# Kernel tuning notes

Measured on AMD Instinct MI355X. Metric: run time of the kernel, lower is better.

Reference implementation:

```python
import jax, jax.numpy as jnp
import numpy as np
from jax import lax

B, S, D = 2, 4096, 1024
E, H, K = 8, 2816, 2  # hidden_dim 4096 -> int(2*4096/3)=2730 -> round up to multiple_of 256 -> 2816


def setup_inputs() -> dict:
    key = jax.random.key(0)
    ks = jax.random.split(key, 5)
    scale = 0.02
    return {
        "x": jax.random.normal(ks[0], (B, S, D), dtype=jnp.float32),
        "router_w": jax.random.normal(ks[1], (E, D), dtype=jnp.float32) * scale,
        "w1": jax.random.normal(ks[2], (E, D, H), dtype=jnp.float32) * scale,
        "w2": jax.random.normal(ks[3], (E, H, D), dtype=jnp.float32) * scale,
        "w3": jax.random.normal(ks[4], (E, D, H), dtype=jnp.float32) * scale,
        "top_k": K,
    }


def reference(x, router_w, w1, w2, w3, top_k):
    b, s, d = x.shape
    e = router_w.shape[0]
    xf = x.reshape(-1, d)                                # [T, D]
    logits = xf @ router_w.T                             # [T, E]
    vals, idx = lax.top_k(logits, top_k)                 # [T, K]
    rw = jax.nn.softmax(vals.astype(jnp.float32), axis=-1).astype(x.dtype)  # [T, K]
    # combine[t, e] = routing weight of expert e for token t (0 if not selected)
    combine = jnp.sum(jax.nn.one_hot(idx, e, dtype=x.dtype) * rw[..., None], axis=1)  # [T, E]

    def body(acc, ew):
        w1e, w2e, w3e, ce = ew                           # [D,H], [H,D], [D,H], [T]
        h = jax.nn.silu(xf @ w1e) * (xf @ w3e)           # SwiGLU FFN, [T, H]
        return acc + (h @ w2e) * ce[:, None], None

    out, _ = lax.scan(body, jnp.zeros_like(xf), (w1, w2, w3, combine.T))
    return out.reshape(b, s, d)
```

## Files before the change

kernel.cpp:

```cpp
#include <hip/hip_runtime.h>
#include <stdint.h>

#define T_TOK 8192
#define DIM   1024
#define NE    8
#define NH    2816
#define NROWS (T_TOK*2)

typedef __attribute__((ext_vector_type(8))) __bf16 bf16x8;
typedef __attribute__((ext_vector_type(4))) float  f32x4;
typedef __attribute__((ext_vector_type(8))) unsigned short ushort8;

typedef __attribute__((address_space(1))) const unsigned int g_as1;
typedef __attribute__((address_space(3))) unsigned int l_as3;
#define GLL(g, l) __builtin_amdgcn_global_load_lds((g_as1*)(g), (l_as3*)(l), 16, 0, 0)
#define MFMA16(a,b,c) __builtin_amdgcn_mfma_f32_16x16x32_bf16(a,b,c,0,0,0)

__device__ __forceinline__ unsigned short f2bf(float f){
  union { float f; uint32_t u; } v; v.f = f;
  uint32_t r = (v.u + 0x7FFFu + ((v.u >> 16) & 1u)) >> 16;
  return (unsigned short)r;
}


__global__ void zero_init_k(float4* __restrict__ out, int* counts, int* cursor){
  if (blockIdx.x == 0 && threadIdx.x < NE){ counts[threadIdx.x] = 0; cursor[threadIdx.x] = 0; }
  int i = blockIdx.x*blockDim.x + threadIdx.x;
  const int n4 = T_TOK*DIM/4;
  const float4 z = make_float4(0.f,0.f,0.f,0.f);
  for (; i < n4; i += gridDim.x*blockDim.x) out[i] = z;
}

__global__ void cvt_k(const float* __restrict__ x, unsigned short* __restrict__ xbf){
  int i = blockIdx.x*blockDim.x + threadIdx.x;
  const int total = T_TOK*DIM/8;
  for (; i < total; i += gridDim.x*blockDim.x){
    const float4 a = *(const float4*)(x + (size_t)i*8);
    const float4 b = *(const float4*)(x + (size_t)i*8 + 4);
    ushort4 lo = make_ushort4(f2bf(a.x), f2bf(a.y), f2bf(a.z), f2bf(a.w));
    ushort4 hi = make_ushort4(f2bf(b.x), f2bf(b.y), f2bf(b.z), f2bf(b.w));
    *(ushort4*)(xbf + (size_t)i*8)     = lo;
    *(ushort4*)(xbf + (size_t)i*8 + 4) = hi;
  }
}


__global__ __launch_bounds__(256) void transpA_k(
    const float* __restrict__ w1, const float* __restrict__ w3,
    const float* __restrict__ w2,
    unsigned short* __restrict__ w1t, unsigned short* __restrict__ w3t,
    unsigned short* __restrict__ w2t, int zbase)
{
  __shared__ unsigned short Tl[64*72];
  const int z = zbase + blockIdx.y;
  const int f = blockIdx.x;
  const size_t DS = (size_t)DIM*NH;
  const float* src; unsigned short* dst; int R, C, rt, ct;
  if (z < 16){
    R = DIM; C = NH; rt = f/44; ct = f - rt*44;
    const int e = z & 7;
    src = (z < 8 ? w1 : w3) + (size_t)e*DS;
    dst = (z < 8 ? w1t : w3t) + (size_t)e*DS;
  } else {
    R = NH; C = DIM; rt = f/16; ct = f - rt*16;
    const int e = z - 16;
    src = w2 + (size_t)e*DS;
    dst = w2t + (size_t)e*DS;
  }
  const int r0 = rt*64, c0 = ct*64;
  const int t = threadIdx.x;
  #pragma unroll
  for (int i=0;i<4;i++){
    const int r  = (t>>4) + i*16;
    const int cq = t & 15;
    const float4 v = *(const float4*)(src + (size_t)(r0+r)*C + c0 + cq*4);
    Tl[(cq*4+0)*72 + r] = f2bf(v.x);
    Tl[(cq*4+1)*72 + r] = f2bf(v.y);
    Tl[(cq*4+2)*72 + r] = f2bf(v.z);
    Tl[(cq*4+3)*72 + r] = f2bf(v.w);
  }
  __syncthreads();
  #pragma unroll
  for (int i=0;i<2;i++){
    const int c  = i*32 + (t>>3);
    const int r8 = (t&7)*8;
    const ushort8 v = *(const ushort8*)&Tl[c*72 + r8];
    *(ushort8*)(dst + (size_t)(c0+c)*R + r0 + r8) = v;
  }
}


__global__ void router_k(const float* __restrict__ x, const float* __restrict__ rw,
                         unsigned short* __restrict__ xbf,
                         int* __restrict__ topk_e, float* __restrict__ topk_w,
                         int* __restrict__ counts){
  const int t = blockIdx.x;
  const int l = threadIdx.x;
  const float* xr = x + (size_t)t * DIM;
  unsigned short* xo = xbf + (size_t)t * DIM;
  float acc[NE];
  #pragma unroll
  for (int e=0;e<NE;e++) acc[e] = 0.f;
  #pragma unroll
  for (int i=0;i<4;i++){
    const int idx = l*4 + i*256;
    const float4 xv = *(const float4*)(xr + idx);
    ushort4 pk = make_ushort4(f2bf(xv.x), f2bf(xv.y), f2bf(xv.z), f2bf(xv.w));
    *(ushort4*)(xo + idx) = pk;
    #pragma unroll
    for (int e=0;e<NE;e++){
      const float4 wv = *(const float4*)(rw + e*DIM + idx);
      acc[e] += xv.x*wv.x + xv.y*wv.y + xv.z*wv.z + xv.w*wv.w;
    }
  }
  #pragma unroll
  for (int e=0;e<NE;e++){
    float v = acc[e];
    #pragma unroll
    for (int off=32; off; off>>=1) v += __shfl_xor(v, off);
    acc[e] = v;
  }
  if (l == 0){
    int e0 = 0; float v0 = acc[0];
    #pragma unroll
    for (int e=1;e<NE;e++) if (acc[e] > v0){ v0 = acc[e]; e0 = e; }
    int e1 = -1; float v1 = -1e30f;
    #pragma unroll
    for (int e=0;e<NE;e++) if (e != e0 && acc[e] > v1){ v1 = acc[e]; e1 = e; }
    float ex = __expf(v1 - v0);
    float s  = 1.f + ex;
    topk_e[t*2]   = e0;  topk_e[t*2+1] = e1;
    topk_w[t*2]   = 1.f/s; topk_w[t*2+1] = ex/s;
    atomicAdd(&counts[e0], 1);
    atomicAdd(&counts[e1], 1);
  }
}

__global__ void prefix_k(const int* __restrict__ counts, int* __restrict__ offs){
  if (threadIdx.x == 0 && blockIdx.x == 0){
    int s = 0;
    for (int e=0;e<NE;e++){ offs[e] = s; s += counts[e]; }
  }
}

__global__ void scatter_k(const int* __restrict__ topk_e, const float* __restrict__ topk_w,
                          const int* __restrict__ offs, int* __restrict__ cursor,
                          int* __restrict__ row_tok, float* __restrict__ row_w){
  int t = blockIdx.x*blockDim.x + threadIdx.x;
  if (t >= T_TOK) return;
  #pragma unroll
  for (int k=0;k<2;k++){
    int e = topk_e[t*2+k];
    int p = atomicAdd(&cursor[e], 1);
    int flat = offs[e] + p;
    row_tok[flat] = t;
    row_w[flat]   = topk_w[t*2+k];
  }
}


__global__ __launch_bounds__(512,2) void gemm1_p(
    const unsigned short* __restrict__ xbf,
    const unsigned short* __restrict__ w1t, const unsigned short* __restrict__ w3t,
    unsigned short* __restrict__ hbuf,
    const int* __restrict__ row_tok,
    const int* __restrict__ counts, const int* __restrict__ offs)
{
  __shared__ unsigned short As [3][128*32];
  __shared__ unsigned short B1s[3][128*32];
  __shared__ unsigned short B3s[3][128*32];

  const int i   = blockIdx.y*64 + blockIdx.x;
  const int lid = (i & 7)*1408 + (i >> 3);
  const int e   = lid / 1408;
  const int rem = lid - e*1408;
  const int h0  = (rem >> 6) * 128;
  const int rb  = rem & 63;

  const int cnt = counts[e];
  const int row0 = rb * 128;
  if (row0 >= cnt) return;
  const int nv   = min(128, cnt - row0);
  const int base = offs[e] + row0;
  const int NK   = DIM/32;

  const int t = threadIdx.x;
  const int r_loc = t >> 2, sct = t & 3;
  const int csw = (sct ^ ((r_loc >> 1) & 3)) * 8;
  const int tok = row_tok[base + min(r_loc, nv-1)];
  const unsigned short* aS  = xbf + (size_t)tok*DIM + csw;
  const unsigned short* b1S = w1t + ((size_t)(e*NH + h0) + r_loc)*DIM + csw;
  const unsigned short* b3S = w3t + ((size_t)(e*NH + h0) + r_loc)*DIM + csw;
  const int lo = t*16;

  const int wid = t >> 6, l = t & 63;
  const int wr = wid >> 2, wc = wid & 3;
  const int lr = l & 15,  lk = l >> 4;
  const int rc = (lk ^ ((lr >> 1) & 3)) * 8;

  f32x4 acc1[4][2], acc3[4][2];
  #pragma unroll
  for (int m=0;m<4;m++)
    #pragma unroll
    for (int n=0;n<2;n++){ acc1[m][n] = (f32x4)0.f; acc3[m][n] = (f32x4)0.f; }

  GLL(aS,    (char*)As[0]+lo); GLL(b1S,    (char*)B1s[0]+lo); GLL(b3S,    (char*)B3s[0]+lo);
  GLL(aS+32, (char*)As[1]+lo); GLL(b1S+32, (char*)B1s[1]+lo); GLL(b3S+32, (char*)B3s[1]+lo);

  for (int kt=0; kt<NK; ++kt){
    if (kt < NK-1) asm volatile("s_waitcnt vmcnt(3)" ::: "memory");
    else           asm volatile("s_waitcnt vmcnt(0)" ::: "memory");
    __builtin_amdgcn_s_barrier();

    if (kt+2 < NK){
      const int kA = (kt+2)*32;
      char* ad  = (char*)As [(kt+2)%3];
      char* b1d = (char*)B1s[(kt+2)%3];
      char* b3d = (char*)B3s[(kt+2)%3];
      GLL(aS+kA, ad+lo); GLL(b1S+kA, b1d+lo); GLL(b3S+kA, b3d+lo);
    }

    const unsigned short* Ab  = As [kt%3];
    const unsigned short* B1b = B1s[kt%3];
    const unsigned short* B3b = B3s[kt%3];

    bf16x8 a[4], b1[2], b3[2];
    #pragma unroll
    for (int m=0;m<4;m++) a[m] = *(const bf16x8*)&Ab[(wr*64 + m*16 + lr)*32 + rc];
    #pragma unroll
    for (int n=0;n<2;n++){
      b1[n] = *(const bf16x8*)&B1b[(wc*32 + n*16 + lr)*32 + rc];
      b3[n] = *(const bf16x8*)&B3b[(wc*32 + n*16 + lr)*32 + rc];
    }
    __builtin_amdgcn_s_setprio(1);
    #pragma unroll
    for (int m=0;m<4;m++)
      #pragma unroll
      for (int n=0;n<2;n++){
        acc1[m][n] = MFMA16(a[m], b1[n], acc1[m][n]);
        acc3[m][n] = MFMA16(a[m], b3[n], acc3[m][n]);
      }
    __builtin_amdgcn_s_setprio(0);
  }

  #pragma unroll
  for (int m=0;m<4;m++){
    #pragma unroll
    for (int i2=0;i2<4;i2++){
      const int r = wr*64 + m*16 + lk*4 + i2;
      if (r < nv){
        const size_t rowbase = (size_t)(base + r) * NH;
        #pragma unroll
        for (int n=0;n<2;n++){
          float z  = acc1[m][n][i2];
          float p3 = acc3[m][n][i2];
          float hv = (z / (1.f + __expf(-z))) * p3;
          hbuf[rowbase + h0 + wc*32 + n*16 + lr] = f2bf(hv);
        }
      }
    }
  }
}

__global__ __launch_bounds__(512,2) void gemm2_p(
    const unsigned short* __restrict__ hbuf,
    const unsigned short* __restrict__ w2t,
    float* __restrict__ out,
    const int* __restrict__ row_tok, const float* __restrict__ row_w,
    const int* __restrict__ counts, const int* __restrict__ offs)
{
  __shared__ unsigned short As[3][128*32];
  __shared__ unsigned short Bs[3][128*32];

  const int i   = blockIdx.y*64 + blockIdx.x;
  const int lid = (i & 7)*512 + (i >> 3);
  const int e   = lid >> 9;
  const int rem = lid & 511;
  const int d0  = (rem >> 6) * 128;
  const int rb  = rem & 63;

  const int cnt = counts[e];
  const int row0 = rb * 128;
  if (row0 >= cnt) return;
  const int nv   = min(128, cnt - row0);
  const int base = offs[e] + row0;
  const int NK   = NH/32;

  const int t = threadIdx.x;
  const int r_loc = t >> 2, sct = t & 3;
  const int csw = (sct ^ ((r_loc >> 1) & 3)) * 8;
  const unsigned short* aS = hbuf + (size_t)(base + min(r_loc, nv-1))*NH + csw;
  const unsigned short* bS = w2t + ((size_t)(e*DIM + d0) + r_loc)*NH + csw;
  const int lo = t*16;

  const int wid = t >> 6, l = t & 63;
  const int wr = wid >> 2, wc = wid & 3;
  const int lr = l & 15,  lk = l >> 4;
  const int rc = (lk ^ ((lr >> 1) & 3)) * 8;

  f32x4 acc[4][2];
  #pragma unroll
  for (int m=0;m<4;m++)
    #pragma unroll
    for (int n=0;n<2;n++) acc[m][n] = (f32x4)0.f;

  GLL(aS,    (char*)As[0]+lo); GLL(bS,    (char*)Bs[0]+lo);
  GLL(aS+32, (char*)As[1]+lo); GLL(bS+32, (char*)Bs[1]+lo);

  for (int kt=0; kt<NK; ++kt){
    if (kt < NK-1) asm volatile("s_waitcnt vmcnt(2)" ::: "memory");
    else           asm volatile("s_waitcnt vmcnt(0)" ::: "memory");
    __builtin_amdgcn_s_barrier();

    if (kt+2 < NK){
      const int kA = (kt+2)*32;
      char* ad = (char*)As[(kt+2)%3];
      char* bd = (char*)Bs[(kt+2)%3];
      GLL(aS+kA, ad+lo); GLL(bS+kA, bd+lo);
    }

    const unsigned short* Ab = As[kt%3];
    const unsigned short* Bb = Bs[kt%3];

    bf16x8 a[4], b[2];
    #pragma unroll
    for (int m=0;m<4;m++) a[m] = *(const bf16x8*)&Ab[(wr*64 + m*16 + lr)*32 + rc];
    #pragma unroll
    for (int n=0;n<2;n++)  b[n] = *(const bf16x8*)&Bb[(wc*32 + n*16 + lr)*32 + rc];
    __builtin_amdgcn_s_setprio(1);
    #pragma unroll
    for (int m=0;m<4;m++)
      #pragma unroll
      for (int n=0;n<2;n++)
        acc[m][n] = MFMA16(a[m], b[n], acc[m][n]);
    __builtin_amdgcn_s_setprio(0);
  }

  #pragma unroll
  for (int m=0;m<4;m++){
    #pragma unroll
    for (int i2=0;i2<4;i2++){
      const int r = wr*64 + m*16 + lk*4 + i2;
      if (r < nv){
        const int flat = base + r;
        const int tok  = row_tok[flat];
        const float wgt = row_w[flat];
        float* orow = out + (size_t)tok * DIM + d0 + wc*32;
        #pragma unroll
        for (int n=0;n<2;n++)
          atomicAdd(&orow[n*16 + lr], acc[m][n][i2] * wgt);
      }
    }
  }
}


__global__ __launch_bounds__(256) void gemm1_k(
    const unsigned short* __restrict__ xbf,
    const float* __restrict__ w1, const float* __restrict__ w3,
    unsigned short* __restrict__ hbuf,
    const int* __restrict__ row_tok,
    const int* __restrict__ counts, const int* __restrict__ offs)
{
  __shared__ unsigned short Al [128*32];
  __shared__ unsigned short B1l[128*32];
  __shared__ unsigned short B3l[128*32];
  const int e   = blockIdx.y >> 6;
  const int rb  = blockIdx.y & 63;
  const int cnt = counts[e];
  const int row0 = rb * 128;
  if (row0 >= cnt) return;
  const int nv   = min(128, cnt - row0);
  const int base = offs[e] + row0;
  const int h0   = blockIdx.x * 128;
  const int t  = threadIdx.x;
  const int ar0 = t >> 2;
  const int ac  = t & 3;
  const int tok0 = row_tok[base + min(ar0,      nv-1)];
  const int tok1 = row_tok[base + min(ar0 + 64, nv-1)];
  const size_t asrc0 = (size_t)tok0 * DIM + ac*8;
  const size_t asrc1 = (size_t)tok1 * DIM + ac*8;
  const int dg = t >> 5;
  const int hq = t & 31;
  const float* w1p = w1 + (size_t)e * DIM * NH + (size_t)(h0 + hq*4);
  const float* w3p = w3 + (size_t)e * DIM * NH + (size_t)(h0 + hq*4);
  const int wid = t >> 6, l = t & 63;
  const int wr = wid >> 1, wc = wid & 1;
  const int lr = l & 15,  lk = l >> 4;
  f32x4 acc1[4][4], acc3[4][4];
  #pragma unroll
  for (int m=0;m<4;m++)
    #pragma unroll
    for (int n=0;n<4;n++){ acc1[m][n] = (f32x4)0.f; acc3[m][n] = (f32x4)0.f; }
  for (int kk=0; kk<DIM/32; ++kk){
    const int k0 = kk*32;
    __syncthreads();
    *(uint4*)&Al[ar0*32 + ac*8]      = *(const uint4*)(xbf + asrc0 + k0);
    *(uint4*)&Al[(ar0+64)*32 + ac*8] = *(const uint4*)(xbf + asrc1 + k0);
    {
      const float4 f0 = *(const float4*)(w1p + (size_t)(k0 + dg*4 + 0)*NH);
      const float4 f1 = *(const float4*)(w1p + (size_t)(k0 + dg*4 + 1)*NH);
      const float4 f2 = *(const float4*)(w1p + (size_t)(k0 + dg*4 + 2)*NH);
      const float4 f3 = *(const float4*)(w1p + (size_t)(k0 + dg*4 + 3)*NH);
      const float* p0=(const float*)&f0; const float* p1=(const float*)&f1;
      const float* p2=(const float*)&f2; const float* p3=(const float*)&f3;
      #pragma unroll
      for (int j=0;j<4;j++){
        ushort4 pk = make_ushort4(f2bf(p0[j]), f2bf(p1[j]), f2bf(p2[j]), f2bf(p3[j]));
        *(ushort4*)&B1l[(hq*4+j)*32 + dg*4] = pk;
      }
      const float4 g0 = *(const float4*)(w3p + (size_t)(k0 + dg*4 + 0)*NH);
      const float4 g1 = *(const float4*)(w3p + (size_t)(k0 + dg*4 + 1)*NH);
      const float4 g2 = *(const float4*)(w3p + (size_t)(k0 + dg*4 + 2)*NH);
      const float4 g3 = *(const float4*)(w3p + (size_t)(k0 + dg*4 + 3)*NH);
      const float* q0=(const float*)&g0; const float* q1=(const float*)&g1;
      const float* q2=(const float*)&g2; const float* q3=(const float*)&g3;
      #pragma unroll
      for (int j=0;j<4;j++){
        ushort4 pk = make_ushort4(f2bf(q0[j]), f2bf(q1[j]), f2bf(q2[j]), f2bf(q3[j]));
        *(ushort4*)&B3l[(hq*4+j)*32 + dg*4] = pk;
      }
    }
    __syncthreads();
    bf16x8 a[4], b1[4], b3[4];
    #pragma unroll
    for (int m=0;m<4;m++) a[m] = *(const bf16x8*)&Al[(wr*64 + m*16 + lr)*32 + lk*8];
    #pragma unroll
    for (int n=0;n<4;n++){
      b1[n] = *(const bf16x8*)&B1l[(wc*64 + n*16 + lr)*32 + lk*8];
      b3[n] = *(const bf16x8*)&B3l[(wc*64 + n*16 + lr)*32 + lk*8];
    }
    #pragma unroll
    for (int m=0;m<4;m++)
      #pragma unroll
      for (int n=0;n<4;n++){
        acc1[m][n] = MFMA16(a[m], b1[n], acc1[m][n]);
        acc3[m][n] = MFMA16(a[m], b3[n], acc3[m][n]);
      }
  }
  #pragma unroll
  for (int m=0;m<4;m++){
    #pragma unroll
    for (int i=0;i<4;i++){
      const int r = wr*64 + m*16 + lk*4 + i;
      if (r < nv){
        const size_t rowbase = (size_t)(base + r) * NH;
        #pragma unroll
        for (int n=0;n<4;n++){
          float z  = acc1[m][n][i];
          float p3 = acc3[m][n][i];
          float hv = (z / (1.f + __expf(-z))) * p3;
          hbuf[rowbase + h0 + wc*64 + n*16 + lr] = f2bf(hv);
        }
      }
    }
  }
}

__global__ __launch_bounds__(256) void gemm2_k(
    const unsigned short* __restrict__ hbuf,
    const float* __restrict__ w2,
    float* __restrict__ out,
    const int* __restrict__ row_tok, const float* __restrict__ row_w,
    const int* __restrict__ counts, const int* __restrict__ offs)
{
  __shared__ unsigned short Al[128*32];
  __shared__ unsigned short Bl[128*32];
  const int e   = blockIdx.y >> 6;
  const int rb  = blockIdx.y & 63;
  const int cnt = counts[e];
  const int row0 = rb * 128;
  if (row0 >= cnt) return;
  const int nv   = min(128, cnt - row0);
  const int base = offs[e] + row0;
  const int d0   = blockIdx.x * 128;
  const int t  = threadIdx.x;
  const int ar0 = t >> 2;
  const int ac  = t & 3;
  const size_t asrc0 = (size_t)(base + min(ar0,      nv-1)) * NH + ac*8;
  const size_t asrc1 = (size_t)(base + min(ar0 + 64, nv-1)) * NH + ac*8;
  const int dg = t >> 5;
  const int hq = t & 31;
  const float* w2p = w2 + (size_t)e * NH * DIM + (size_t)(d0 + hq*4);
  const int wid = t >> 6, l = t & 63;
  const int wr = wid >> 1, wc = wid & 1;
  const int lr = l & 15,  lk = l >> 4;
  f32x4 acc[4][4];
  #pragma unroll
  for (int m=0;m<4;m++)
    #pragma unroll
    for (int n=0;n<4;n++) acc[m][n] = (f32x4)0.f;
  for (int kk=0; kk<NH/32; ++kk){
    const int k0 = kk*32;
    __syncthreads();
    *(uint4*)&Al[ar0*32 + ac*8]      = *(const uint4*)(hbuf + asrc0 + k0);
    *(uint4*)&Al[(ar0+64)*32 + ac*8] = *(const uint4*)(hbuf + asrc1 + k0);
    {
      const float4 f0 = *(const float4*)(w2p + (size_t)(k0 + dg*4 + 0)*DIM);
      const float4 f1 = *(const float4*)(w2p + (size_t)(k0 + dg*4 + 1)*DIM);
      const float4 f2 = *(const float4*)(w2p + (size_t)(k0 + dg*4 + 2)*DIM);
      const float4 f3 = *(const float4*)(w2p + (size_t)(k0 + dg*4 + 3)*DIM);
      const float* p0=(const float*)&f0; const float* p1=(const float*)&f1;
      const float* p2=(const float*)&f2; const float* p3=(const float*)&f3;
      #pragma unroll
      for (int j=0;j<4;j++){
        ushort4 pk = make_ushort4(f2bf(p0[j]), f2bf(p1[j]), f2bf(p2[j]), f2bf(p3[j]));
        *(ushort4*)&Bl[(hq*4+j)*32 + dg*4] = pk;
      }
    }
    __syncthreads();
    bf16x8 a[4], b[4];
    #pragma unroll
    for (int m=0;m<4;m++) a[m] = *(const bf16x8*)&Al[(wr*64 + m*16 + lr)*32 + lk*8];
    #pragma unroll
    for (int n=0;n<4;n++)  b[n] = *(const bf16x8*)&Bl[(wc*64 + n*16 + lr)*32 + lk*8];
    #pragma unroll
    for (int m=0;m<4;m++)
      #pragma unroll
      for (int n=0;n<4;n++)
        acc[m][n] = MFMA16(a[m], b[n], acc[m][n]);
  }
  #pragma unroll
  for (int m=0;m<4;m++){
    #pragma unroll
    for (int i=0;i<4;i++){
      const int r = wr*64 + m*16 + lk*4 + i;
      if (r < nv){
        const int flat = base + r;
        const int tok  = row_tok[flat];
        const float wgt = row_w[flat];
        float* orow = out + (size_t)tok * DIM + d0 + wc*64;
        #pragma unroll
        for (int n=0;n<4;n++)
          atomicAdd(&orow[n*16 + lr], acc[m][n][i] * wgt);
      }
    }
  }
}


extern "C" void kernel_launch(void* const* d_in, const int* in_sizes, int n_in,
                              void* d_out, int out_size, void* d_ws, size_t ws_size,
                              hipStream_t stream) {
  (void)in_sizes; (void)n_in; (void)out_size;
  const float* x   = (const float*)d_in[0];
  const float* rw  = (const float*)d_in[1];
  const float* w1  = (const float*)d_in[2];
  const float* w2  = (const float*)d_in[3];
  const float* w3  = (const float*)d_in[4];
  float* out = (float*)d_out;
  char* ws = (char*)d_ws;

  const size_t SZ_XBF  = (size_t)T_TOK*DIM*2;
  const size_t SZ_HBUF = (size_t)NROWS*NH*2;
  const size_t SZ_WT   = (size_t)NE*NH*DIM*2;
  const size_t SZ_SMALL = (size_t)NROWS*4*2 + (size_t)T_TOK*2*4*2 + 3*64*4 + 4096;
  const size_t NEED_FAST = SZ_XBF + SZ_HBUF + 2*SZ_WT + SZ_SMALL;
  const size_t NEED_FULL = SZ_XBF + SZ_HBUF + 3*SZ_WT + SZ_SMALL;

  if (ws_size >= NEED_FAST) {
    const bool full = (ws_size >= NEED_FULL);
    size_t off = 0;
    unsigned short* xbf  = (unsigned short*)(ws + off); off += SZ_XBF;
    unsigned short* hbuf = (unsigned short*)(ws + off); off += SZ_HBUF;
    unsigned short* w1t  = (unsigned short*)(ws + off); off += SZ_WT;
    unsigned short* w3t  = (unsigned short*)(ws + off); off += SZ_WT;
    unsigned short* w2t;
    if (full){ w2t = (unsigned short*)(ws + off); off += SZ_WT; }
    else      { w2t = w1t; }
    int*   row_tok = (int*)  (ws + off); off += NROWS*4;
    float* row_w   = (float*)(ws + off); off += NROWS*4;
    int*   topk_e  = (int*)  (ws + off); off += T_TOK*2*4;
    float* topk_w  = (float*)(ws + off); off += T_TOK*2*4;
    int*   counts  = (int*)  (ws + off); off += 64;
    int*   offs    = (int*)  (ws + off); off += 64;
    int*   cursor  = (int*)  (ws + off); off += 64;

    zero_init_k<<<2048, 256, 0, stream>>>((float4*)out, counts, cursor);
    router_k   <<<T_TOK, 64, 0, stream>>>(x, rw, xbf, topk_e, topk_w, counts);
    prefix_k   <<<1, 64, 0, stream>>>(counts, offs);
    scatter_k  <<<(T_TOK+255)/256, 256, 0, stream>>>(topk_e, topk_w, offs, cursor, row_tok, row_w);
    if (full){
      transpA_k <<<dim3(704, 24), 256, 0, stream>>>(w1, w3, w2, w1t, w3t, w2t, 0);
      gemm1_p   <<<dim3(64, 176), 512, 0, stream>>>(xbf, w1t, w3t, hbuf, row_tok, counts, offs);
      gemm2_p   <<<dim3(64, NE*8), 512, 0, stream>>>(hbuf, w2t, out, row_tok, row_w, counts, offs);
    } else {
      transpA_k <<<dim3(704, 16), 256, 0, stream>>>(w1, w3, w2, w1t, w3t, w2t, 0);
      gemm1_p   <<<dim3(64, 176), 512, 0, stream>>>(xbf, w1t, w3t, hbuf, row_tok, counts, offs);
      transpA_k <<<dim3(704, 8), 256, 0, stream>>>(w1, w3, w2, w1t, w3t, w2t, 16);
      gemm2_p   <<<dim3(64, NE*8), 512, 0, stream>>>(hbuf, w2t, out, row_tok, row_w, counts, offs);
    }
  } else {
    size_t off = 0;
    unsigned short* xbf  = (unsigned short*)(ws + off); off += SZ_XBF;
    unsigned short* hbuf = (unsigned short*)(ws + off); off += SZ_HBUF;
    int*   row_tok = (int*)  (ws + off); off += NROWS*4;
    float* row_w   = (float*)(ws + off); off += NROWS*4;
    int*   topk_e  = (int*)  (ws + off); off += T_TOK*2*4;
    float* topk_w  = (float*)(ws + off); off += T_TOK*2*4;
    int*   counts  = (int*)  (ws + off); off += 64;
    int*   offs    = (int*)  (ws + off); off += 64;
    int*   cursor  = (int*)  (ws + off); off += 64;

    zero_init_k<<<2048, 256, 0, stream>>>((float4*)out, counts, cursor);
    router_k   <<<T_TOK, 64, 0, stream>>>(x, rw, xbf, topk_e, topk_w, counts);
    prefix_k   <<<1, 64, 0, stream>>>(counts, offs);
    scatter_k  <<<(T_TOK+255)/256, 256, 0, stream>>>(topk_e, topk_w, offs, cursor, row_tok, row_w);
    gemm1_k    <<<dim3(NH/128, NE*64), 256, 0, stream>>>(xbf, w1, w3, hbuf, row_tok, counts, offs);
    gemm2_k    <<<dim3(DIM/128, NE*64), 256, 0, stream>>>(hbuf, w2, out, row_tok, row_w, counts, offs);
  }
}
```

Measured before the change: 751.4 us.

## Widen gemm2 K-tile to 64 with double-buffered LDS and 8-way swizzle

The second expert GEMM moves from a triple-buffered K-step of 32 to a double-buffered K-step of 64. Each thread issues two global-to-LDS loads per operand per stage, and the LDS swizzle changes to an XOR over 8 chunks. The aim is to halve the number of barrier and wait iterations and run more MFMAs per synchronization. The cost is a full vmcnt(0) wait each iteration, which gives less prefetch depth. LDS use rises from 48KB to 64KB per block, which may affect occupancy at two blocks per CU.

New measurement: 766.4 us. +2.0%, slower.

```diff
diff --git a/kernel.cpp b/kernel.cpp
--- a/kernel.cpp
+++ b/kernel.cpp
@@ -262,15 +262,15 @@
   }
 }
 
-__global__ __launch_bounds__(512,2) void gemm2_p(
+__global__ __launch_bounds__(512,2) void gemm2_v(
     const unsigned short* __restrict__ hbuf,
     const unsigned short* __restrict__ w2t,
     float* __restrict__ out,
     const int* __restrict__ row_tok, const float* __restrict__ row_w,
     const int* __restrict__ counts, const int* __restrict__ offs)
 {
-  __shared__ unsigned short As[3][128*32];
-  __shared__ unsigned short Bs[3][128*32];
+  __shared__ unsigned short As[2][128*64];
+  __shared__ unsigned short Bs[2][128*64];
 
   const int i   = blockIdx.y*64 + blockIdx.x;
   const int lid = (i & 7)*512 + (i >> 3);
@@ -284,19 +284,20 @@
   if (row0 >= cnt) return;
   const int nv   = min(128, cnt - row0);
   const int base = offs[e] + row0;
-  const int NK   = NH/32;
-
-  const int t = threadIdx.x;
-  const int r_loc = t >> 2, sct = t & 3;
-  const int csw = (sct ^ ((r_loc >> 1) & 3)) * 8;
-  const unsigned short* aS = hbuf + (size_t)(base + min(r_loc, nv-1))*NH + csw;
-  const unsigned short* bS = w2t + ((size_t)(e*DIM + d0) + r_loc)*NH + csw;
-  const int lo = t*16;
+  const int NK   = NH/64;
+
+  const int t  = threadIdx.x;
+  const int r8 = t >> 3, sl = t & 7;
+  const int csw = ((sl ^ (r8 & 7)) << 3);
+  const unsigned short* aP0 = hbuf + (size_t)(base + min(r8,      nv-1))*NH + csw;
+  const unsigned short* aP1 = hbuf + (size_t)(base + min(r8 + 64, nv-1))*NH + csw;
+  const unsigned short* bP0 = w2t + ((size_t)(e*DIM + d0) + r8)*NH + csw;
+  const unsigned short* bP1 = bP0 + (size_t)64*NH;
+  const int lo0 = t*16, lo1 = 8192 + t*16;
 
   const int wid = t >> 6, l = t & 63;
   const int wr = wid >> 2, wc = wid & 3;
   const int lr = l & 15,  lk = l >> 4;
-  const int rc = (lk ^ ((lr >> 1) & 3)) * 8;
 
   f32x4 acc[4][2];
   #pragma unroll
@@ -304,35 +305,52 @@
     #pragma unroll
     for (int n=0;n<2;n++) acc[m][n] = (f32x4)0.f;
 
-  GLL(aS,    (char*)As[0]+lo); GLL(bS,    (char*)Bs[0]+lo);
-  GLL(aS+32, (char*)As[1]+lo); GLL(bS+32, (char*)Bs[1]+lo);
+  GLL(aP0, (char*)As[0]+lo0); GLL(aP1, (char*)As[0]+lo1);
+  GLL(bP0, (char*)Bs[0]+lo0); GLL(bP1, (char*)Bs[0]+lo1);
 
   for (int kt=0; kt<NK; ++kt){
-    if (kt < NK-1) asm volatile("s_waitcnt vmcnt(2)" ::: "memory");
-    else           asm volatile("s_waitcnt vmcnt(0)" ::: "memory");
+    const int cur = kt & 1;
+    asm volatile("s_waitcnt vmcnt(0)" ::: "memory");
     __builtin_amdgcn_s_barrier();
 
-    if (kt+2 < NK){
-      const int kA = (kt+2)*32;
-      char* ad = (char*)As[(kt+2)%3];
-      char* bd = (char*)Bs[(kt+2)%3];
-      GLL(aS+kA, ad+lo); GLL(bS+kA, bd+lo);
-    }
-
-    const unsigned short* Ab = As[kt%3];
-    const unsigned short* Bb = Bs[kt%3];
-
-    bf16x8 a[4], b[2];
-    #pragma unroll
-    for (int m=0;m<4;m++) a[m] = *(const bf16x8*)&Ab[(wr*64 + m*16 + lr)*32 + rc];
-    #pragma unroll
-    for (int n=0;n<2;n++)  b[n] = *(const bf16x8*)&Bb[(wc*32 + n*16 + lr)*32 + rc];
+    if (kt+1 < NK){
+      const int kof = (kt+1)*64;
+      char* ad = (char*)As[cur^1];
+      char* bd = (char*)Bs[cur^1];
+      GLL(aP0+kof, ad+lo0); GLL(aP1+kof, ad+lo1);
+      GLL(bP0+kof, bd+lo0); GLL(bP1+kof, bd+lo1);
+    }
+
+    const unsigned short* Ab = As[cur];
+    const unsigned short* Bb = Bs[cur];
+
+    bf16x8 a[4][2], b[2][2];
+    #pragma unroll
+    for (int m=0;m<4;m++){
+      const int row = wr*64 + m*16 + lr;
+      #pragma unroll
+      for (int ks=0;ks<2;ks++){
+        const int ck = ks*4 + lk;
+        a[m][ks] = *(const bf16x8*)&Ab[row*64 + ((ck ^ (row & 7)) << 3)];
+      }
+    }
+    #pragma unroll
+    for (int n=0;n<2;n++){
+      const int row = wc*32 + n*16 + lr;
+      #pragma unroll
+      for (int ks=0;ks<2;ks++){
+        const int ck = ks*4 + lk;
+        b[n][ks] = *(const bf16x8*)&Bb[row*64 + ((ck ^ (row & 7)) << 3)];
+      }
+    }
     __builtin_amdgcn_s_setprio(1);
     #pragma unroll
-    for (int m=0;m<4;m++)
-      #pragma unroll
-      for (int n=0;n<2;n++)
-        acc[m][n] = MFMA16(a[m], b[n], acc[m][n]);
+    for (int ks=0;ks<2;ks++)
+      #pragma unroll
+      for (int m=0;m<4;m++)
+        #pragma unroll
+        for (int n=0;n<2;n++)
+          acc[m][n] = MFMA16(a[m][ks], b[n][ks], acc[m][n]);
     __builtin_amdgcn_s_setprio(0);
   }
 
@@ -583,12 +601,12 @@
     if (full){
       transpA_k <<<dim3(704, 24), 256, 0, stream>>>(w1, w3, w2, w1t, w3t, w2t, 0);
       gemm1_p   <<<dim3(64, 176), 512, 0, stream>>>(xbf, w1t, w3t, hbuf, row_tok, counts, offs);
-      gemm2_p   <<<dim3(64, NE*8), 512, 0, stream>>>(hbuf, w2t, out, row_tok, row_w, counts, offs);
+      gemm2_v   <<<dim3(64, NE*8), 512, 0, stream>>>(hbuf, w2t, out, row_tok, row_w, counts, offs);
     } else {
       transpA_k <<<dim3(704, 16), 256, 0, stream>>>(w1, w3, w2, w1t, w3t, w2t, 0);
       gemm1_p   <<<dim3(64, 176), 512, 0, stream>>>(xbf, w1t, w3t, hbuf, row_tok, counts, offs);
       transpA_k <<<dim3(704, 8), 256, 0, stream>>>(w1, w3, w2, w1t, w3t, w2t, 16);
-      gemm2_p   <<<dim3(64, NE*8), 512, 0, stream>>>(hbuf, w2t, out, row_tok, row_w, counts, offs);
+      gemm2_v   <<<dim3(64, NE*8), 512, 0, stream>>>(hbuf, w2t, out, row_tok, row_w, counts, offs);
     }
   } else {
     size_t off = 0;
```
